# Optimization experiments

Measured on AMD Instinct MI355X. Metric: run time of the kernel, lower is better.

Reference implementation:

```python
import jax, jax.numpy as jnp
import numpy as np

B, L, K = 2, 1024, 30
NUM_RBF = 16
MAX_REL = 32  # max_relative_feature
POS_DIM = 16

# atom order in stacked table: N=0, Ca=1, C=2, O=3, Cb=4
_PAIRS = [(0,0),(2,2),(3,3),(4,4),(1,0),(1,2),(1,3),(1,4),(0,2),(0,3),(0,4),
          (4,2),(4,3),(3,2),(0,1),(2,1),(3,1),(4,1),(2,0),(3,0),(4,0),(2,4),(3,4),(2,3)]


def setup_inputs() -> dict:
    key = jax.random.key(0)
    ks = jax.random.split(key, 6)
    X = jax.random.normal(ks[0], (B, L, 4, 3), dtype=jnp.float32) * 3.0
    chain_idx = jnp.sort(jax.random.randint(ks[1], (B, L), 0, 4), axis=-1)
    mask = jnp.ones((B, L), dtype=jnp.float32)
    E_idx = jax.random.randint(ks[2], (B, L, K), 0, L)
    D_neighbors = jax.random.uniform(ks[3], (B, L, K), dtype=jnp.float32) * 22.0
    W_pos = jax.random.normal(ks[4], (POS_DIM, 2 * MAX_REL + 2), dtype=jnp.float32) * 0.1
    b_pos = jax.random.normal(ks[5], (POS_DIM,), dtype=jnp.float32) * 0.01
    return {"X": X, "chain_idx": chain_idx, "mask": mask, "E_idx": E_idx,
            "D_neighbors": D_neighbors, "W_pos": W_pos, "b_pos": b_pos}


def _rbf(D):
    # D: [..., ] -> [..., NUM_RBF]
    D_mu = jnp.linspace(2.0, 22.0, NUM_RBF, dtype=D.dtype)
    D_sigma = (22.0 - 2.0) / NUM_RBF
    return jnp.exp(-(((D[..., None] - D_mu) / D_sigma) ** 2))


def _residue_idx(chain_idx):
    # faithful to the torch loop: chains 0..n-2 get 100*(chain#) + global pos, last chain stays -100
    boundary = jnp.concatenate(
        [jnp.zeros((chain_idx.shape[0], 1), jnp.int32),
         (chain_idx[:, 1:] != chain_idx[:, :-1]).astype(jnp.int32)], axis=1)
    chain_num = jnp.cumsum(boundary, axis=1)              # [B,L]
    last = chain_num[:, -1:]
    pos = jnp.arange(chain_idx.shape[1], dtype=jnp.int32)[None, :]
    return jnp.where(chain_num < last, 100 * chain_num + pos, -100)


def _forward(X, chain_idx, mask, E_idx, D_neighbors, W_pos, b_pos):
    N, Ca, C, O = X[:, :, 0], X[:, :, 1], X[:, :, 2], X[:, :, 3]
    b = Ca - N
    c = C - Ca
    a = jnp.cross(b, c)
    Cb = -0.58273431 * a + 0.56802827 * b - 0.54067466 * c + Ca
    atoms = jnp.stack([N, Ca, C, O, Cb], axis=0)          # [5,B,L,3]

    ia = jnp.array([p[0] for p in _PAIRS])
    ib = jnp.array([p[1] for p in _PAIRS])

    def pair_rbf(A_pts, B_pts):
        # full pairwise distance then gather down to top-k neighbors (faithful to original)
        dX = A_pts[:, :, None, :] - B_pts[:, None, :, :]   # [B,L,L,3]
        D = jnp.sqrt(jnp.sum(dX ** 2, axis=-1) + 1e-6)     # [B,L,L]
        Dn = jnp.take_along_axis(D, E_idx, axis=2)         # [B,L,K]
        return _rbf(Dn)                                     # [B,L,K,16]

    RBF_pairs = jax.vmap(pair_rbf)(atoms[ia], atoms[ib])   # [24,B,L,K,16]
    RBF_pairs = jnp.transpose(RBF_pairs, (1, 2, 3, 0, 4)).reshape(
        X.shape[0], X.shape[1], E_idx.shape[2], 24 * NUM_RBF)
    RBF_all = jnp.concatenate([_rbf(D_neighbors), RBF_pairs], axis=-1)  # [B,L,K,400]

    ridx = _residue_idx(chain_idx)                          # [B,L] int32
    offset = ridx[:, :, None] - ridx[:, None, :]            # [B,L,L]
    offset = jnp.take_along_axis(offset, E_idx, axis=2)     # [B,L,K]
    d_chains = (chain_idx[:, :, None] == chain_idx[:, None, :]).astype(jnp.int32)
    E_chains = jnp.take_along_axis(d_chains, E_idx, axis=2)  # [B,L,K]

    d = jnp.clip(offset + MAX_REL, 0, 2 * MAX_REL) * E_chains + (1 - E_chains) * (2 * MAX_REL + 1)
    d_onehot = jax.nn.one_hot(d, 2 * MAX_REL + 2, dtype=W_pos.dtype)   # [B,L,K,66]
    E_positional = jnp.einsum('blkc,ec->blke', d_onehot, W_pos) + b_pos

    return jnp.concatenate([E_positional, RBF_all], axis=-1)  # [B,L,K,416]


def reference(X, chain_idx, mask, E_idx, D_neighbors, W_pos, b_pos):
    return _forward(X, chain_idx, mask, E_idx, D_neighbors, W_pos, b_pos)
```

## Files before the change

kernel.cpp:

```cpp
#include <hip/hip_runtime.h>

#define BB 2
#define LL 1024
#define KK 30
#define NCH 416
#define PER_BLOCK (KK * NCH)
#define NF4 (PER_BLOCK / 4)

typedef float floatx4 __attribute__((ext_vector_type(4)));

__device__ __constant__ unsigned char PAIR_A[24] =
    {0,2,3,4,1,1,1,1,0,0,0,4,4,3,0,2,3,4,2,3,4,2,3,2};
__device__ __constant__ unsigned char PAIR_B[24] =
    {0,2,3,4,0,2,3,4,2,3,4,2,3,2,1,1,1,1,0,0,0,4,4,3};

__global__ __launch_bounds__(256)
void feat_fused(const float* __restrict__ X, const int* __restrict__ chainG,
                const int* __restrict__ E_idx, const float* __restrict__ D_neighbors,
                const float* __restrict__ W_pos, const float* __restrict__ b_pos,
                float* __restrict__ out)
{
    __shared__ float Wst[16 * 66];
    __shared__ float latm[16];
    __shared__ float natm[KK][16];
    __shared__ float pd[KK][26];
    __shared__ int   dd[KK];
    __shared__ int   iaib[24];
    __shared__ int   wmask[4];

    const int tid = threadIdx.x;
    const int bi  = blockIdx.x;
    const int l   = bi & (LL - 1);
    const int rowbase = bi - l;

    const int4 cv = reinterpret_cast<const int4*>(chainG + rowbase)[tid];
    int pm = (1 << cv.x) | (1 << cv.y) | (1 << cv.z) | (1 << cv.w);
    #pragma unroll
    for (int off = 32; off >= 1; off >>= 1) pm |= __shfl_xor(pm, off, 64);
    if ((tid & 63) == 0) wmask[tid >> 6] = pm;

    for (int i = tid; i < 16 * 66; i += 256) Wst[i] = W_pos[i] + b_pos[i / 66];
    if (tid < 24) iaib[tid] = ((int)(3 * PAIR_A[tid]) << 8) | (int)(3 * PAIR_B[tid]);

    int jj = 0, chj = 0;
    if (tid < KK) {
        jj  = E_idx[bi * KK + tid];
        chj = chainG[rowbase + jj];
        pd[tid][0] = D_neighbors[bi * KK + tid] * 0.8f;
    }
    if (tid <= KK) {
        const int j = (tid < KK) ? (rowbase + jj) : bi;
        const float4* xp = reinterpret_cast<const float4*>(X + (size_t)j * 12);
        const float4 x0 = xp[0], x1 = xp[1], x2 = xp[2];
        const float bx = x0.w - x0.x, by = x1.x - x0.y, bz = x1.y - x0.z;
        const float cx = x1.z - x0.w, cy = x1.w - x1.x, cz = x2.x - x1.y;
        const float ax = by * cz - bz * cy;
        const float ay = bz * cx - bx * cz;
        const float az = bx * cy - by * cx;
        const float ka = -0.58273431f, kb = 0.56802827f, kc = -0.54067466f;
        float* ap = (tid < KK) ? &natm[tid][0] : &latm[0];
        ap[0]  = x0.x; ap[1]  = x0.y; ap[2]  = x0.z;
        ap[3]  = x0.w; ap[4]  = x1.x; ap[5]  = x1.y;
        ap[6]  = x1.z; ap[7]  = x1.w; ap[8]  = x2.x;
        ap[9]  = x2.y; ap[10] = x2.z; ap[11] = x2.w;
        ap[12] = ka * ax + kb * bx + kc * cx + x0.w;
        ap[13] = ka * ay + kb * by + kc * cy + x1.x;
        ap[14] = ka * az + kb * bz + kc * cz + x1.y;
    }
    __syncthreads();

    if (tid < KK) {
        const int mask = wmask[0] | wmask[1] | wmask[2] | wmask[3];
        const int chl  = chainG[bi];
        const int npres = __popc(mask);
        const int cl1 = __popc(mask & ((2 << chl) - 1));
        const int cj1 = __popc(mask & ((2 << chj) - 1));
        const int rl = (cl1 < npres) ? (100 * (cl1 - 1) + l)  : -100;
        const int rj = (cj1 < npres) ? (100 * (cj1 - 1) + jj) : -100;
        int off = rl - rj + 32;
        off = off < 0 ? 0 : (off > 64 ? 64 : off);
        dd[tid] = (chl == chj) ? off : 65;
    }

    for (int i = tid; i < KK * 24; i += 256) {
        const int k  = i / 24;
        const int p  = i - k * 24;
        const int pk = iaib[p];
        const int ao = pk >> 8;
        const int bo = pk & 255;
        const float dx = latm[ao]     - natm[k][bo];
        const float dy = latm[ao + 1] - natm[k][bo + 1];
        const float dz = latm[ao + 2] - natm[k][bo + 2];
        const float D  = sqrtf(dx * dx + dy * dy + dz * dz + 1e-6f);
        pd[k][1 + p] = D * 0.8f;
    }
    __syncthreads();

    float* outp = out + (size_t)bi * PER_BLOCK;
    const float MU0    = 1.6f;
    const float MUSTEP = 1.0666666666666667f;
    const float NLOG2E = -1.44269504088896f;

    #pragma unroll 1
    for (int i4 = tid; i4 < NF4; i4 += 256) {
        const int k  = i4 / 104;
        const int c0 = (i4 - k * 104) * 4;
        floatx4 v;
        if (c0 < 16) {
            const int d = dd[k];
            v.x = Wst[(c0 + 0) * 66 + d];
            v.y = Wst[(c0 + 1) * 66 + d];
            v.z = Wst[(c0 + 2) * 66 + d];
            v.w = Wst[(c0 + 3) * 66 + d];
        } else {
            const int q  = (c0 - 16) >> 4;
            const int m0 = (c0 - 16) & 15;
            const float D8 = pd[k][q];
            const float mu = MU0 + (float)m0 * MUSTEP;
            const float t0 = D8 - mu;
            const float t1 = D8 - (mu + MUSTEP);
            const float t2 = D8 - (mu + 2.0f * MUSTEP);
            const float t3 = D8 - (mu + 3.0f * MUSTEP);
            v.x = __builtin_amdgcn_exp2f(t0 * t0 * NLOG2E);
            v.y = __builtin_amdgcn_exp2f(t1 * t1 * NLOG2E);
            v.z = __builtin_amdgcn_exp2f(t2 * t2 * NLOG2E);
            v.w = __builtin_amdgcn_exp2f(t3 * t3 * NLOG2E);
        }
        __builtin_nontemporal_store(v, reinterpret_cast<floatx4*>(outp + i4 * 4));
    }
}

extern "C" void kernel_launch(void* const* d_in, const int* in_sizes, int n_in,
                              void* d_out, int out_size, void* d_ws, size_t ws_size,
                              hipStream_t stream)
{
    const float* X           = (const float*)d_in[0];
    const int*   chain_idx   = (const int*)  d_in[1];
    const int*   E_idx       = (const int*)  d_in[3];
    const float* D_neighbors = (const float*)d_in[4];
    const float* W_pos       = (const float*)d_in[5];
    const float* b_pos       = (const float*)d_in[6];
    float* out = (float*)d_out;

    feat_fused<<<BB * LL, 256, 0, stream>>>(X, chain_idx, E_idx, D_neighbors,
                                            W_pos, b_pos, out);
}
```

Baseline: 26.47 us.

## Fuse pair-distance computation into RBF output loop with per-thread distance ownership

Removes the separate pair-distance pass and its shared-memory staging. Each thread now computes one distance and writes all 16 RBF values for it as four float4 stores, with positional entries handled as separate work items. This drops one phase of work and reduces the shared-memory round trip. In exchange, each thread's stores become strided 64-byte chunks rather than fully coalesced consecutive float4s, the nontemporal store hint is gone, and loads are less balanced because 870 items are spread over 256 threads.

New measurement: 39.83 us. 50.5% more time.

```diff
diff --git a/kernel.cpp b/kernel.cpp
--- a/kernel.cpp
+++ b/kernel.cpp
@@ -5,9 +5,9 @@
 #define KK 30
 #define NCH 416
 #define PER_BLOCK (KK * NCH)
-#define NF4 (PER_BLOCK / 4)
-
-typedef float floatx4 __attribute__((ext_vector_type(4)));
+#define NRBF_ITEM (KK * 25)
+#define NPOS_ITEM (KK * 4)
+#define NITEMS (NRBF_ITEM + NPOS_ITEM)
 
 __device__ __constant__ unsigned char PAIR_A[24] =
     {0,2,3,4,1,1,1,1,0,0,0,4,4,3,0,2,3,4,2,3,4,2,3,2};
@@ -15,15 +15,15 @@
     {0,2,3,4,0,2,3,4,2,3,4,2,3,2,1,1,1,1,0,0,0,4,4,3};
 
 __global__ __launch_bounds__(256)
-void feat_fused(const float* __restrict__ X, const int* __restrict__ chainG,
-                const int* __restrict__ E_idx, const float* __restrict__ D_neighbors,
-                const float* __restrict__ W_pos, const float* __restrict__ b_pos,
-                float* __restrict__ out)
+void feat_own(const float* __restrict__ X, const int* __restrict__ chainG,
+              const int* __restrict__ E_idx, const float* __restrict__ D_neighbors,
+              const float* __restrict__ W_pos, const float* __restrict__ b_pos,
+              float* __restrict__ out)
 {
     __shared__ float Wst[16 * 66];
     __shared__ float latm[16];
     __shared__ float natm[KK][16];
-    __shared__ float pd[KK][26];
+    __shared__ float dnb[KK];
     __shared__ int   dd[KK];
     __shared__ int   iaib[24];
     __shared__ int   wmask[4];
@@ -46,7 +46,7 @@
     if (tid < KK) {
         jj  = E_idx[bi * KK + tid];
         chj = chainG[rowbase + jj];
-        pd[tid][0] = D_neighbors[bi * KK + tid] * 0.8f;
+        dnb[tid] = D_neighbors[bi * KK + tid] * 0.8f;
     }
     if (tid <= KK) {
         const int j = (tid < KK) ? (rowbase + jj) : bi;
@@ -81,19 +81,6 @@
         off = off < 0 ? 0 : (off > 64 ? 64 : off);
         dd[tid] = (chl == chj) ? off : 65;
     }
-
-    for (int i = tid; i < KK * 24; i += 256) {
-        const int k  = i / 24;
-        const int p  = i - k * 24;
-        const int pk = iaib[p];
-        const int ao = pk >> 8;
-        const int bo = pk & 255;
-        const float dx = latm[ao]     - natm[k][bo];
-        const float dy = latm[ao + 1] - natm[k][bo + 1];
-        const float dz = latm[ao + 2] - natm[k][bo + 2];
-        const float D  = sqrtf(dx * dx + dy * dy + dz * dz + 1e-6f);
-        pd[k][1 + p] = D * 0.8f;
-    }
     __syncthreads();
 
     float* outp = out + (size_t)bi * PER_BLOCK;
@@ -102,31 +89,49 @@
     const float NLOG2E = -1.44269504088896f;
 
     #pragma unroll 1
-    for (int i4 = tid; i4 < NF4; i4 += 256) {
-        const int k  = i4 / 104;
-        const int c0 = (i4 - k * 104) * 4;
-        floatx4 v;
-        if (c0 < 16) {
-            const int d = dd[k];
+    for (int it = tid; it < NITEMS; it += 256) {
+        if (it < NRBF_ITEM) {
+            const int k = it / 25;
+            const int r = it - k * 25;
+            float D8;
+            if (r == 0) {
+                D8 = dnb[k];
+            } else {
+                const int pk = iaib[r - 1];
+                const int ao = pk >> 8;
+                const int bo = pk & 255;
+                const float dx = latm[ao]     - natm[k][bo];
+                const float dy = latm[ao + 1] - natm[k][bo + 1];
+                const float dz = latm[ao + 2] - natm[k][bo + 2];
+                D8 = sqrtf(dx * dx + dy * dy + dz * dz + 1e-6f) * 0.8f;
+            }
+            float* op = outp + k * NCH + 16 + r * 16;
+            #pragma unroll
+            for (int g = 0; g < 4; ++g) {
+                const float mu = MU0 + (float)(g * 4) * MUSTEP;
+                const float t0 = D8 - mu;
+                const float t1 = D8 - (mu + MUSTEP);
+                const float t2 = D8 - (mu + 2.0f * MUSTEP);
+                const float t3 = D8 - (mu + 3.0f * MUSTEP);
+                float4 v;
+                v.x = __builtin_amdgcn_exp2f(t0 * t0 * NLOG2E);
+                v.y = __builtin_amdgcn_exp2f(t1 * t1 * NLOG2E);
+                v.z = __builtin_amdgcn_exp2f(t2 * t2 * NLOG2E);
+                v.w = __builtin_amdgcn_exp2f(t3 * t3 * NLOG2E);
+                *reinterpret_cast<float4*>(op + g * 4) = v;
+            }
+        } else {
+            const int p  = it - NRBF_ITEM;
+            const int k  = p >> 2;
+            const int c0 = (p & 3) * 4;
+            const int d  = dd[k];
+            float4 v;
             v.x = Wst[(c0 + 0) * 66 + d];
             v.y = Wst[(c0 + 1) * 66 + d];
             v.z = Wst[(c0 + 2) * 66 + d];
             v.w = Wst[(c0 + 3) * 66 + d];
-        } else {
-            const int q  = (c0 - 16) >> 4;
-            const int m0 = (c0 - 16) & 15;
-            const float D8 = pd[k][q];
-            const float mu = MU0 + (float)m0 * MUSTEP;
-            const float t0 = D8 - mu;
-            const float t1 = D8 - (mu + MUSTEP);
-            const float t2 = D8 - (mu + 2.0f * MUSTEP);
-            const float t3 = D8 - (mu + 3.0f * MUSTEP);
-            v.x = __builtin_amdgcn_exp2f(t0 * t0 * NLOG2E);
-            v.y = __builtin_amdgcn_exp2f(t1 * t1 * NLOG2E);
-            v.z = __builtin_amdgcn_exp2f(t2 * t2 * NLOG2E);
-            v.w = __builtin_amdgcn_exp2f(t3 * t3 * NLOG2E);
+            *reinterpret_cast<float4*>(outp + k * NCH + c0) = v;
         }
-        __builtin_nontemporal_store(v, reinterpret_cast<floatx4*>(outp + i4 * 4));
     }
 }
 
@@ -142,6 +147,6 @@
     const float* b_pos       = (const float*)d_in[6];
     float* out = (float*)d_out;
 
-    feat_fused<<<BB * LL, 256, 0, stream>>>(X, chain_idx, E_idx, D_neighbors,
-                                            W_pos, b_pos, out);
+    feat_own<<<BB * LL, 256, 0, stream>>>(X, chain_idx, E_idx, D_neighbors,
+                                          W_pos, b_pos, out);
 }
```

## Process four positions per block with register prefetch of next position's gathers

Applied to the files above, without the earlier changes.

Each block now handles four consecutive residue positions instead of one, amortising the W_pos table staging and chain-mask reduction across them. The gathers for the next position (neighbour indices, distances, coordinates) are issued into registers before the current position's distance and RBF work, so their latency can overlap compute. The output store also changes from a nontemporal store to a plain float4 store. In exchange, the grid shrinks to a quarter of the blocks and each position adds extra barriers, which may reduce latency hiding across the device.

Measured after the change: 26.53 us. Within noise of the previous version (+0.2%).

```diff
diff --git a/kernel.cpp b/kernel.cpp
--- a/kernel.cpp
+++ b/kernel.cpp
@@ -4,10 +4,9 @@
 #define LL 1024
 #define KK 30
 #define NCH 416
-#define PER_BLOCK (KK * NCH)
-#define NF4 (PER_BLOCK / 4)
-
-typedef float floatx4 __attribute__((ext_vector_type(4)));
+#define PER_POS (KK * NCH)
+#define NF4 (PER_POS / 4)
+#define PPB 4
 
 __device__ __constant__ unsigned char PAIR_A[24] =
     {0,2,3,4,1,1,1,1,0,0,0,4,4,3,0,2,3,4,2,3,4,2,3,2};
@@ -15,10 +14,10 @@
     {0,2,3,4,0,2,3,4,2,3,4,2,3,2,1,1,1,1,0,0,0,4,4,3};
 
 __global__ __launch_bounds__(256)
-void feat_fused(const float* __restrict__ X, const int* __restrict__ chainG,
-                const int* __restrict__ E_idx, const float* __restrict__ D_neighbors,
-                const float* __restrict__ W_pos, const float* __restrict__ b_pos,
-                float* __restrict__ out)
+void feat_pipe(const float* __restrict__ X, const int* __restrict__ chainG,
+               const int* __restrict__ E_idx, const float* __restrict__ D_neighbors,
+               const float* __restrict__ W_pos, const float* __restrict__ b_pos,
+               float* __restrict__ out)
 {
     __shared__ float Wst[16 * 66];
     __shared__ float latm[16];
@@ -28,10 +27,9 @@
     __shared__ int   iaib[24];
     __shared__ int   wmask[4];
 
-    const int tid = threadIdx.x;
-    const int bi  = blockIdx.x;
-    const int l   = bi & (LL - 1);
-    const int rowbase = bi - l;
+    const int tid  = threadIdx.x;
+    const int pos0 = blockIdx.x * PPB;
+    const int rowbase = pos0 & ~(LL - 1);
 
     const int4 cv = reinterpret_cast<const int4*>(chainG + rowbase)[tid];
     int pm = (1 << cv.x) | (1 << cv.y) | (1 << cv.z) | (1 << cv.w);
@@ -42,91 +40,109 @@
     for (int i = tid; i < 16 * 66; i += 256) Wst[i] = W_pos[i] + b_pos[i / 66];
     if (tid < 24) iaib[tid] = ((int)(3 * PAIR_A[tid]) << 8) | (int)(3 * PAIR_B[tid]);
 
-    int jj = 0, chj = 0;
-    if (tid < KK) {
-        jj  = E_idx[bi * KK + tid];
-        chj = chainG[rowbase + jj];
-        pd[tid][0] = D_neighbors[bi * KK + tid] * 0.8f;
-    }
-    if (tid <= KK) {
-        const int j = (tid < KK) ? (rowbase + jj) : bi;
-        const float4* xp = reinterpret_cast<const float4*>(X + (size_t)j * 12);
-        const float4 x0 = xp[0], x1 = xp[1], x2 = xp[2];
-        const float bx = x0.w - x0.x, by = x1.x - x0.y, bz = x1.y - x0.z;
-        const float cx = x1.z - x0.w, cy = x1.w - x1.x, cz = x2.x - x1.y;
-        const float ax = by * cz - bz * cy;
-        const float ay = bz * cx - bx * cz;
-        const float az = bx * cy - by * cx;
-        const float ka = -0.58273431f, kb = 0.56802827f, kc = -0.54067466f;
-        float* ap = (tid < KK) ? &natm[tid][0] : &latm[0];
-        ap[0]  = x0.x; ap[1]  = x0.y; ap[2]  = x0.z;
-        ap[3]  = x0.w; ap[4]  = x1.x; ap[5]  = x1.y;
-        ap[6]  = x1.z; ap[7]  = x1.w; ap[8]  = x2.x;
-        ap[9]  = x2.y; ap[10] = x2.z; ap[11] = x2.w;
-        ap[12] = ka * ax + kb * bx + kc * cx + x0.w;
-        ap[13] = ka * ay + kb * by + kc * cy + x1.x;
-        ap[14] = ka * az + kb * bz + kc * cz + x1.y;
-    }
+    int   jj = 0, chj = 0, chl = 0;
+    float dnbr = 0.0f;
+    float4 x0, x1, x2;
+
+    auto prefetch = [&](int pos) {
+        if (tid < KK) {
+            jj   = E_idx[pos * KK + tid];
+            dnbr = D_neighbors[pos * KK + tid] * 0.8f;
+            chj  = chainG[rowbase + jj];
+        }
+        if (tid <= KK) {
+            const int j = (tid < KK) ? (rowbase + jj) : pos;
+            const float4* xp = reinterpret_cast<const float4*>(X + (size_t)j * 12);
+            x0 = xp[0]; x1 = xp[1]; x2 = xp[2];
+        }
+        chl = chainG[pos];
+    };
+    prefetch(pos0);
     __syncthreads();
 
-    if (tid < KK) {
-        const int mask = wmask[0] | wmask[1] | wmask[2] | wmask[3];
-        const int chl  = chainG[bi];
-        const int npres = __popc(mask);
-        const int cl1 = __popc(mask & ((2 << chl) - 1));
-        const int cj1 = __popc(mask & ((2 << chj) - 1));
-        const int rl = (cl1 < npres) ? (100 * (cl1 - 1) + l)  : -100;
-        const int rj = (cj1 < npres) ? (100 * (cj1 - 1) + jj) : -100;
-        int off = rl - rj + 32;
-        off = off < 0 ? 0 : (off > 64 ? 64 : off);
-        dd[tid] = (chl == chj) ? off : 65;
-    }
-
-    for (int i = tid; i < KK * 24; i += 256) {
-        const int k  = i / 24;
-        const int p  = i - k * 24;
-        const int pk = iaib[p];
-        const int ao = pk >> 8;
-        const int bo = pk & 255;
-        const float dx = latm[ao]     - natm[k][bo];
-        const float dy = latm[ao + 1] - natm[k][bo + 1];
-        const float dz = latm[ao + 2] - natm[k][bo + 2];
-        const float D  = sqrtf(dx * dx + dy * dy + dz * dz + 1e-6f);
-        pd[k][1 + p] = D * 0.8f;
-    }
-    __syncthreads();
-
-    float* outp = out + (size_t)bi * PER_BLOCK;
     const float MU0    = 1.6f;
     const float MUSTEP = 1.0666666666666667f;
     const float NLOG2E = -1.44269504088896f;
 
-    #pragma unroll 1
-    for (int i4 = tid; i4 < NF4; i4 += 256) {
-        const int k  = i4 / 104;
-        const int c0 = (i4 - k * 104) * 4;
-        floatx4 v;
-        if (c0 < 16) {
-            const int d = dd[k];
-            v.x = Wst[(c0 + 0) * 66 + d];
-            v.y = Wst[(c0 + 1) * 66 + d];
-            v.z = Wst[(c0 + 2) * 66 + d];
-            v.w = Wst[(c0 + 3) * 66 + d];
-        } else {
-            const int q  = (c0 - 16) >> 4;
-            const int m0 = (c0 - 16) & 15;
-            const float D8 = pd[k][q];
-            const float mu = MU0 + (float)m0 * MUSTEP;
-            const float t0 = D8 - mu;
-            const float t1 = D8 - (mu + MUSTEP);
-            const float t2 = D8 - (mu + 2.0f * MUSTEP);
-            const float t3 = D8 - (mu + 3.0f * MUSTEP);
-            v.x = __builtin_amdgcn_exp2f(t0 * t0 * NLOG2E);
-            v.y = __builtin_amdgcn_exp2f(t1 * t1 * NLOG2E);
-            v.z = __builtin_amdgcn_exp2f(t2 * t2 * NLOG2E);
-            v.w = __builtin_amdgcn_exp2f(t3 * t3 * NLOG2E);
+    for (int p = 0; p < PPB; ++p) {
+        const int bi = pos0 + p;
+        const int l  = bi & (LL - 1);
+
+        if (tid <= KK) {
+            const float bx = x0.w - x0.x, by = x1.x - x0.y, bz = x1.y - x0.z;
+            const float cx = x1.z - x0.w, cy = x1.w - x1.x, cz = x2.x - x1.y;
+            const float ax = by * cz - bz * cy;
+            const float ay = bz * cx - bx * cz;
+            const float az = bx * cy - by * cx;
+            const float ka = -0.58273431f, kb = 0.56802827f, kc = -0.54067466f;
+            float* ap = (tid < KK) ? &natm[tid][0] : &latm[0];
+            ap[0]  = x0.x; ap[1]  = x0.y; ap[2]  = x0.z;
+            ap[3]  = x0.w; ap[4]  = x1.x; ap[5]  = x1.y;
+            ap[6]  = x1.z; ap[7]  = x1.w; ap[8]  = x2.x;
+            ap[9]  = x2.y; ap[10] = x2.z; ap[11] = x2.w;
+            ap[12] = ka * ax + kb * bx + kc * cx + x0.w;
+            ap[13] = ka * ay + kb * by + kc * cy + x1.x;
+            ap[14] = ka * az + kb * bz + kc * cz + x1.y;
         }
-        __builtin_nontemporal_store(v, reinterpret_cast<floatx4*>(outp + i4 * 4));
+        if (tid < KK) {
+            pd[tid][0] = dnbr;
+            const int mask  = wmask[0] | wmask[1] | wmask[2] | wmask[3];
+            const int npres = __popc(mask);
+            const int cl1 = __popc(mask & ((2 << chl) - 1));
+            const int cj1 = __popc(mask & ((2 << chj) - 1));
+            const int rl = (cl1 < npres) ? (100 * (cl1 - 1) + l)  : -100;
+            const int rj = (cj1 < npres) ? (100 * (cj1 - 1) + jj) : -100;
+            int off = rl - rj + 32;
+            off = off < 0 ? 0 : (off > 64 ? 64 : off);
+            dd[tid] = (chl == chj) ? off : 65;
+        }
+        __syncthreads();
+
+        if (p + 1 < PPB) prefetch(bi + 1);
+
+        for (int i = tid; i < KK * 24; i += 256) {
+            const int k  = i / 24;
+            const int pp = i - k * 24;
+            const int pk = iaib[pp];
+            const int ao = pk >> 8;
+            const int bo = pk & 255;
+            const float dx = latm[ao]     - natm[k][bo];
+            const float dy = latm[ao + 1] - natm[k][bo + 1];
+            const float dz = latm[ao + 2] - natm[k][bo + 2];
+            const float D  = sqrtf(dx * dx + dy * dy + dz * dz + 1e-6f);
+            pd[k][1 + pp] = D * 0.8f;
+        }
+        __syncthreads();
+
+        float* outp = out + (size_t)bi * PER_POS;
+        #pragma unroll 1
+        for (int i4 = tid; i4 < NF4; i4 += 256) {
+            const int k  = i4 / 104;
+            const int c0 = (i4 - k * 104) * 4;
+            float4 v;
+            if (c0 < 16) {
+                const int d = dd[k];
+                v.x = Wst[(c0 + 0) * 66 + d];
+                v.y = Wst[(c0 + 1) * 66 + d];
+                v.z = Wst[(c0 + 2) * 66 + d];
+                v.w = Wst[(c0 + 3) * 66 + d];
+            } else {
+                const int q  = (c0 - 16) >> 4;
+                const int m0 = (c0 - 16) & 15;
+                const float D8 = pd[k][q];
+                const float mu = MU0 + (float)m0 * MUSTEP;
+                const float t0 = D8 - mu;
+                const float t1 = D8 - (mu + MUSTEP);
+                const float t2 = D8 - (mu + 2.0f * MUSTEP);
+                const float t3 = D8 - (mu + 3.0f * MUSTEP);
+                v.x = __builtin_amdgcn_exp2f(t0 * t0 * NLOG2E);
+                v.y = __builtin_amdgcn_exp2f(t1 * t1 * NLOG2E);
+                v.z = __builtin_amdgcn_exp2f(t2 * t2 * NLOG2E);
+                v.w = __builtin_amdgcn_exp2f(t3 * t3 * NLOG2E);
+            }
+            *reinterpret_cast<float4*>(outp + i4 * 4) = v;
+        }
+        __syncthreads();
     }
 }
 
@@ -142,6 +158,6 @@
     const float* b_pos       = (const float*)d_in[6];
     float* out = (float*)d_out;
 
-    feat_fused<<<BB * LL, 256, 0, stream>>>(X, chain_idx, E_idx, D_neighbors,
-                                            W_pos, b_pos, out);
+    feat_pipe<<<(BB * LL) / PPB, 256, 0, stream>>>(X, chain_idx, E_idx,
+                                                   D_neighbors, W_pos, b_pos, out);
 }
```
